# Performance work log

Hardware: AMD Instinct MI355X
Metric: run time of the kernel (lower is better)

## Reference

```python
import jax, jax.numpy as jnp
import numpy as np

ATOM_VOC = 128
APO = 128
NHEAD = 16
D_MODEL = 512
BOND_VOC = 32
CHIRAL_VOC = 4
B, L = 4, 384


def setup_inputs() -> dict:
    key = jax.random.key(0)
    ks = jax.random.split(key, 12)
    atoms = jax.random.randint(ks[0], (B, L), 0, ATOM_VOC)
    chirals = jax.random.randint(ks[1], (B, L), 0, CHIRAL_VOC)
    coordinates = jax.random.normal(ks[2], (B, L, 3), dtype=jnp.float32)
    bonds = jax.random.randint(ks[3], (B, L, L), 0, BOND_VOC)
    # embedding tables; padding_idx rows (0) zeroed to match torch padding_idx
    atype_emb = jax.random.normal(ks[4], (ATOM_VOC, D_MODEL), dtype=jnp.float32) * 0.02
    atype_emb = atype_emb.at[0].set(0.0)
    chiral_emb = jax.random.normal(ks[5], (CHIRAL_VOC, D_MODEL), dtype=jnp.float32) * 0.02
    chiral_emb = chiral_emb.at[0].set(0.0)
    apair_w_emb = jax.random.normal(ks[6], (ATOM_VOC * ATOM_VOC, APO), dtype=jnp.float32) * 0.02
    apair_b_emb = jax.random.normal(ks[7], (ATOM_VOC * ATOM_VOC, APO), dtype=jnp.float32) * 0.02
    means = jax.random.normal(ks[8], (APO,), dtype=jnp.float32) * 0.1
    stds = jnp.ones((APO,), dtype=jnp.float32) + jax.random.normal(ks[9], (APO,), dtype=jnp.float32) * 0.1
    bond_emb = jax.random.normal(ks[10], (BOND_VOC, NHEAD), dtype=jnp.float32) * 0.02
    bond_emb = bond_emb.at[0].set(0.0)
    lin_w = jax.random.normal(ks[11], (NHEAD, APO), dtype=jnp.float32) * (1.0 / np.sqrt(APO))
    lin_b = jnp.zeros((NHEAD,), dtype=jnp.float32)
    return dict(atoms=atoms, chirals=chirals, coordinates=coordinates, bonds=bonds,
                atype_emb=atype_emb, chiral_emb=chiral_emb,
                apair_w_emb=apair_w_emb, apair_b_emb=apair_b_emb,
                means=means, stds=stds, bond_emb=bond_emb, lin_w=lin_w, lin_b=lin_b)


def reference(atoms, chirals, coordinates, bonds, atype_emb, chiral_emb,
              apair_w_emb, apair_b_emb, means, stds, bond_emb, lin_w, lin_b):
    # atoms: [b,l] int; coordinates: [b,l,3]; bonds: [b,l,l] int
    atoms_emb = atype_emb[atoms] + chiral_emb[chirals]          # [b,l,d]
    atoms_emb = jnp.transpose(atoms_emb, (1, 0, 2))             # [l,b,d]
    diff = coordinates[:, None, :, :] - coordinates[:, :, None, :]  # [b,l,l,3]
    d2 = jnp.sum(diff * diff, axis=-1)
    distances = jnp.sqrt(d2 + 1e-12)                            # [b,l,l] (eps avoids nan grad on diag)
    apair_idx = atoms[:, None, :] * ATOM_VOC + atoms[:, :, None]  # [b,l,l]
    ap = apair_w_emb[apair_idx] * distances[..., None] + apair_b_emb[apair_idx]  # [b,l,l,apo]
    s = jnp.abs(stds) + 1e-5
    ap = jnp.exp(-0.5 * jnp.square((ap - means) / s)) / (np.sqrt(2 * np.pi) * s)
    ap = jnp.einsum('bijk,hk->bijh', ap, lin_w) + lin_b + bond_emb[bonds]  # [b,l,l,nhead]
    pad = (atoms == 0)[:, None, :, None]                        # mask key atoms (dim 2)
    ap = jnp.where(pad, -jnp.inf, ap)
    ap = jnp.transpose(ap, (0, 3, 1, 2))                        # [b,nhead,l,l]
    return atoms_emb, ap
```

## Files before the change

### kernel.cpp

```cpp
#include <hip/hip_runtime.h>
#include <hip/hip_fp16.h>
#include <math.h>
#include <string.h>

#define ATOM_VOC 128
#define APO      128
#define NHEAD    16
#define D_MODEL  512
#define NB       4
#define NL       384

typedef __attribute__((ext_vector_type(8))) _Float16 f16x8;
typedef __attribute__((ext_vector_type(4))) float    f32x4;
typedef __attribute__((ext_vector_type(4))) unsigned u32x4;

#define PACK_DWORDS (ATOM_VOC * ATOM_VOC * APO)
#define BFT_SHORTS  (4 * 4 * 16 * 8)

static __device__ inline unsigned short f2h(float x) {
    __half h = __float2half(x);
    unsigned short u; memcpy(&u, &h, 2); return u;
}

__global__ __launch_bounds__(128) void pack_kernel(
    const float* __restrict__ apw, const float* __restrict__ apb,
    const float* __restrict__ means, const float* __restrict__ stds,
    const float* __restrict__ lin_w,
    unsigned* __restrict__ pack, unsigned short* __restrict__ bft, int write_bft)
{
    const int t    = threadIdx.x;
    const int v    = blockIdx.x;
    const int ai   = blockIdx.y;
    const int half = t >> 6;
    const int p    = t & 63;
    const int k0   = 2 * p, k1 = 2 * p + 1;

    const float s0  = fabsf(stds[k0]) + 1e-5f;
    const float s1  = fabsf(stds[k1]) + 1e-5f;
    const float ag0 = 0.84932180028802f / s0;
    const float ag1 = 0.84932180028802f / s1;

    const size_t srcrow = ((size_t)v * ATOM_VOC + ai) * APO;
    float x0, x1;
    if (half == 0) {
        x0 = apw[srcrow + k0] * ag0;
        x1 = apw[srcrow + k1] * ag1;
    } else {
        x0 = (apb[srcrow + k0] - means[k0]) * ag0;
        x1 = (apb[srcrow + k1] - means[k1]) * ag1;
    }
    const int dst = (p >> 5) * 64 + half * 32 + (p & 31);
    pack[((size_t)ai * ATOM_VOC + v) * APO + dst] =
        ((unsigned)f2h(x1) << 16) | f2h(x0);

    if (write_bft && v == 0 && ai == 0) {
#pragma unroll
        for (int hh = 0; hh < 2; ++hh) {
            const int cid  = t + hh * 128;
            const int ks   = cid >> 6;
            const int quad = (cid >> 4) & 3;
            const int h    = cid & 15;
            const int kb   = ks * 32 + quad * 8;
            unsigned short tmp[8];
#pragma unroll
            for (int u = 0; u < 8; ++u) {
                const int kk = kb + u;
                float z = 0.3989422804014327f / (fabsf(stds[kk]) + 1e-5f);
                tmp[u] = f2h(lin_w[h * APO + kk] * z);
            }
            memcpy(&bft[(size_t)cid * 8], tmp, 16);
        }
    }
}

__global__ __launch_bounds__(256) void atoms_emb_kernel(
    const int* __restrict__ atoms, const int* __restrict__ chirals,
    const float* __restrict__ atype_emb, const float* __restrict__ chiral_emb,
    float* __restrict__ out)
{
    const int D4 = D_MODEL / 4;
    int t = blockIdx.x * 256 + threadIdx.x;
    if (t >= NL * NB * D4) return;
    int d4 = t % D4;
    int bl = t / D4;
    int b  = bl % NB;
    int l  = bl / NB;
    int a  = atoms[b * NL + l];
    int c  = chirals[b * NL + l];
    float4 va = ((const float4*)(atype_emb  + (size_t)a * D_MODEL))[d4];
    float4 vc = ((const float4*)(chiral_emb + (size_t)c * D_MODEL))[d4];
    float4 o;
    o.x = va.x + vc.x; o.y = va.y + vc.y; o.z = va.z + vc.z; o.w = va.w + vc.w;
    ((float4*)out)[t] = o;
}

__global__ __launch_bounds__(512, 8) void ap_kernel(
    const int*            __restrict__ atoms,
    const float*          __restrict__ coords,
    const int*            __restrict__ bonds,
    const unsigned*       __restrict__ pack,
    const unsigned short* __restrict__ bft,
    const float*          __restrict__ bond_emb,
    const float*          __restrict__ lin_b,
    float*                __restrict__ out)
{
    const int i    = blockIdx.x;
    const int b    = blockIdx.y;
    const int t    = threadIdx.x;
    const int lane = t & 63;
    const int wave = t >> 6;
    const int h    = lane & 15;
    const int quad = lane >> 4;

    __shared__ unsigned tbl[ATOM_VOC * 64];

    const int ai = atoms[b * NL + i];
    const unsigned* src = pack + (size_t)ai * (ATOM_VOC * APO);

    f16x8 bfrag[4];
#pragma unroll
    for (int ks = 0; ks < 4; ++ks)
        memcpy(&bfrag[ks], bft + ((size_t)((ks * 4 + quad) * 16 + h)) * 8, 16);
    const float lbh = lin_b[h];

    const float cix = coords[((size_t)b * NL + i) * 3 + 0];
    const float ciy = coords[((size_t)b * NL + i) * 3 + 1];
    const float ciz = coords[((size_t)b * NL + i) * 3 + 2];

    int     jv[3];
    __half2 jd2[3];
#pragma unroll
    for (int it = 0; it < 3; ++it) {
        const int j = it * 128 + wave * 16 + h;
        jv[it] = atoms[b * NL + j];
        const float dx = coords[((size_t)b * NL + j) * 3 + 0] - cix;
        const float dy = coords[((size_t)b * NL + j) * 3 + 1] - ciy;
        const float dz = coords[((size_t)b * NL + j) * 3 + 2] - ciz;
        jd2[it] = __half2half2(__float2half(
            sqrtf(fmaf(dx, dx, fmaf(dy, dy, dz * dz)) + 1e-12f)));
    }

    f32x4 acc[3] = {{0.f,0.f,0.f,0.f},{0.f,0.f,0.f,0.f},{0.f,0.f,0.f,0.f}};

#pragma unroll
    for (int ph = 0; ph < 2; ++ph) {
        if (ph) __syncthreads();
#pragma unroll
        for (int itx = 0; itx < 4; ++itx) {
            int c   = itx * 512 + t;
            int row = c >> 4;
            int cc  = c & 15;
            u32x4 d = ((const u32x4*)src)[row * 32 + ph * 16 + cc];
            *(u32x4*)&tbl[row * 64 + 4 * (cc ^ (row & 15))] = d;
        }
        __syncthreads();

#pragma unroll
        for (int it = 0; it < 3; ++it) {
            const int v  = jv[it];
            const int vb = v * 64;
            const int vx = v & 15;
            const __half2 d2 = jd2[it];
#pragma unroll
            for (int ks2 = 0; ks2 < 2; ++ks2) {
                const u32x4 wch = *(const u32x4*)&tbl[vb + 4 * ((ks2 * 4 + quad) ^ vx)];
                const u32x4 bch = *(const u32x4*)&tbl[vb + 4 * ((8 + ks2 * 4 + quad) ^ vx)];
                unsigned afw[4];
#pragma unroll
                for (int q = 0; q < 4; ++q) {
                    __half2 w2, b2;
                    unsigned wd = wch[q], bd = bch[q];
                    memcpy(&w2, &wd, 4); memcpy(&b2, &bd, 4);
                    __half2 u2  = __hfma2(w2, d2, b2);
                    __half2 nm2 = __hmul2(u2, __hneg2(u2));
                    __half2 g2  = h2exp2(nm2);
                    memcpy(&afw[q], &g2, 4);
                }
                f16x8 af;
                memcpy(&af, afw, 16);
                acc[it] = __builtin_amdgcn_mfma_f32_16x16x32_f16(
                    af, bfrag[ph * 2 + ks2], acc[it], 0, 0, 0);
            }
        }
    }

    const size_t bondrow = ((size_t)b * NL + i) * NL;
    float* op = out + (((size_t)(b * NHEAD + h)) * NL + i) * NL;
#pragma unroll
    for (int it = 0; it < 3; ++it) {
        const int jb = it * 128 + wave * 16 + quad * 4;
#pragma unroll
        for (int r = 0; r < 4; ++r) {
            const int bidx = bonds[bondrow + jb + r];
            const int ajr  = atoms[b * NL + jb + r];
            float vv = acc[it][r] + lbh + bond_emb[bidx * NHEAD + h];
            if (ajr == 0) vv = -1.0e30f;
            op[jb + r] = vv;
        }
    }
}

extern "C" void kernel_launch(void* const* d_in, const int* in_sizes, int n_in,
                              void* d_out, int out_size, void* d_ws, size_t ws_size,
                              hipStream_t stream)
{
    const int*   atoms      = (const int*)d_in[0];
    const int*   chirals    = (const int*)d_in[1];
    const float* coords     = (const float*)d_in[2];
    const int*   bonds      = (const int*)d_in[3];
    const float* atype_emb  = (const float*)d_in[4];
    const float* chiral_emb = (const float*)d_in[5];
    const float* apw        = (const float*)d_in[6];
    const float* apb        = (const float*)d_in[7];
    const float* means      = (const float*)d_in[8];
    const float* stds       = (const float*)d_in[9];
    const float* bond_emb   = (const float*)d_in[10];
    const float* lin_w      = (const float*)d_in[11];
    const float* lin_b      = (const float*)d_in[12];
    float* out = (float*)d_out;

    unsigned* pack = (unsigned*)d_ws;
    unsigned short* bftp = (unsigned short*)((char*)d_ws + (size_t)PACK_DWORDS * 4);

    pack_kernel<<<dim3(ATOM_VOC, ATOM_VOC), dim3(128), 0, stream>>>(
        apw, apb, means, stds, lin_w, pack, bftp, 1);

    {
        const int total = NL * NB * (D_MODEL / 4);
        atoms_emb_kernel<<<dim3((total + 255) / 256), dim3(256), 0, stream>>>(
            atoms, chirals, atype_emb, chiral_emb, out);
    }
    {
        float* out2 = out + (size_t)NL * NB * D_MODEL;
        ap_kernel<<<dim3(NL, NB), dim3(512), 0, stream>>>(
            atoms, coords, bonds, pack, bftp, bond_emb, lin_b, out2);
    }
}
```

Measured before the change: 136.9 us.

## Vectorize pack kernel, fuse atom embedding into ap kernel, use direct LDS loads

Rewrites the pack kernel so each thread converts eight values with float4 loads and writes a 16-byte packed chunk, reducing scalar memory traffic. Folds the atom-embedding gather into ap_kernel to drop a separate launch. Stages the pair table into LDS with global_load_lds, issued early so it overlaps setup work. Vectorizes the final bond/mask output stores. These add complexity in the LDS addressing and swizzle mapping.

Measured after the change: 131.8 us. 3.7% less time.

```diff
diff --git a/kernel.cpp b/kernel.cpp
--- a/kernel.cpp
+++ b/kernel.cpp
@@ -22,87 +22,85 @@
     unsigned short u; memcpy(&u, &h, 2); return u;
 }
 
-__global__ __launch_bounds__(128) void pack_kernel(
+static __device__ inline void gload_lds16(const void* g, void* l) {
+    __builtin_amdgcn_global_load_lds(
+        (const __attribute__((address_space(1))) void*)g,
+        (__attribute__((address_space(3))) void*)l, 16, 0, 0);
+}
+
+__global__ __launch_bounds__(256) void pack_kernel(
     const float* __restrict__ apw, const float* __restrict__ apb,
     const float* __restrict__ means, const float* __restrict__ stds,
     const float* __restrict__ lin_w,
     unsigned* __restrict__ pack, unsigned short* __restrict__ bft, int write_bft)
 {
-    const int t    = threadIdx.x;
-    const int v    = blockIdx.x;
-    const int ai   = blockIdx.y;
-    const int half = t >> 6;
-    const int p    = t & 63;
-    const int k0   = 2 * p, k1 = 2 * p + 1;
-
-    const float s0  = fabsf(stds[k0]) + 1e-5f;
-    const float s1  = fabsf(stds[k1]) + 1e-5f;
-    const float ag0 = 0.84932180028802f / s0;
-    const float ag1 = 0.84932180028802f / s1;
+    const int t     = threadIdx.x;
+    const int r     = t >> 5;
+    const int u     = t & 31;
+    const int ph    = u >> 4;
+    const int half  = (u >> 3) & 1;
+    const int q     = u & 7;
+    const int rowid = blockIdx.x * 8 + r;
+    const int ai    = rowid >> 7;
+    const int v     = rowid & 127;
+    const int kb    = ph * 64 + q * 8;
 
     const size_t srcrow = ((size_t)v * ATOM_VOC + ai) * APO;
-    float x0, x1;
-    if (half == 0) {
-        x0 = apw[srcrow + k0] * ag0;
-        x1 = apw[srcrow + k1] * ag1;
-    } else {
-        x0 = (apb[srcrow + k0] - means[k0]) * ag0;
-        x1 = (apb[srcrow + k1] - means[k1]) * ag1;
-    }
-    const int dst = (p >> 5) * 64 + half * 32 + (p & 31);
-    pack[((size_t)ai * ATOM_VOC + v) * APO + dst] =
-        ((unsigned)f2h(x1) << 16) | f2h(x0);
-
-    if (write_bft && v == 0 && ai == 0) {
-#pragma unroll
-        for (int hh = 0; hh < 2; ++hh) {
-            const int cid  = t + hh * 128;
-            const int ks   = cid >> 6;
-            const int quad = (cid >> 4) & 3;
-            const int h    = cid & 15;
-            const int kb   = ks * 32 + quad * 8;
-            unsigned short tmp[8];
-#pragma unroll
-            for (int u = 0; u < 8; ++u) {
-                const int kk = kb + u;
-                float z = 0.3989422804014327f / (fabsf(stds[kk]) + 1e-5f);
-                tmp[u] = f2h(lin_w[h * APO + kk] * z);
-            }
-            memcpy(&bft[(size_t)cid * 8], tmp, 16);
+    const float* sp = (half ? apb : apw) + srcrow + kb;
+    const float4 f0  = *(const float4*)(sp);
+    const float4 f1  = *(const float4*)(sp + 4);
+    const float4 sd0 = *(const float4*)(stds + kb);
+    const float4 sd1 = *(const float4*)(stds + kb + 4);
+
+    float x[8]  = {f0.x, f0.y, f0.z, f0.w, f1.x, f1.y, f1.z, f1.w};
+    float ss[8] = {sd0.x, sd0.y, sd0.z, sd0.w, sd1.x, sd1.y, sd1.z, sd1.w};
+    if (half) {
+        const float4 m0 = *(const float4*)(means + kb);
+        const float4 m1 = *(const float4*)(means + kb + 4);
+        const float mm[8] = {m0.x, m0.y, m0.z, m0.w, m1.x, m1.y, m1.z, m1.w};
+#pragma unroll
+        for (int j = 0; j < 8; ++j) x[j] = x[j] - mm[j];
+    }
+    unsigned dw[4];
+#pragma unroll
+    for (int j = 0; j < 4; ++j) {
+        const float ag0 = 0.84932180028802f / (fabsf(ss[2 * j])     + 1e-5f);
+        const float ag1 = 0.84932180028802f / (fabsf(ss[2 * j + 1]) + 1e-5f);
+        dw[j] = ((unsigned)f2h(x[2 * j + 1] * ag1) << 16) | f2h(x[2 * j] * ag0);
+    }
+    const int dst = ph * 64 + half * 32 + q * 4;
+    *(u32x4*)&pack[((size_t)ai * ATOM_VOC + v) * APO + dst] = *(const u32x4*)dw;
+
+    if (write_bft && blockIdx.x == 0) {
+        const int cid  = t;
+        const int ks   = cid >> 6;
+        const int quad = (cid >> 4) & 3;
+        const int hh   = cid & 15;
+        const int kb2  = ks * 32 + quad * 8;
+        unsigned short tmp[8];
+#pragma unroll
+        for (int uu = 0; uu < 8; ++uu) {
+            const int kk = kb2 + uu;
+            float z = 0.3989422804014327f / (fabsf(stds[kk]) + 1e-5f);
+            tmp[uu] = f2h(lin_w[hh * APO + kk] * z);
         }
-    }
-}
-
-__global__ __launch_bounds__(256) void atoms_emb_kernel(
-    const int* __restrict__ atoms, const int* __restrict__ chirals,
-    const float* __restrict__ atype_emb, const float* __restrict__ chiral_emb,
-    float* __restrict__ out)
-{
-    const int D4 = D_MODEL / 4;
-    int t = blockIdx.x * 256 + threadIdx.x;
-    if (t >= NL * NB * D4) return;
-    int d4 = t % D4;
-    int bl = t / D4;
-    int b  = bl % NB;
-    int l  = bl / NB;
-    int a  = atoms[b * NL + l];
-    int c  = chirals[b * NL + l];
-    float4 va = ((const float4*)(atype_emb  + (size_t)a * D_MODEL))[d4];
-    float4 vc = ((const float4*)(chiral_emb + (size_t)c * D_MODEL))[d4];
-    float4 o;
-    o.x = va.x + vc.x; o.y = va.y + vc.y; o.z = va.z + vc.z; o.w = va.w + vc.w;
-    ((float4*)out)[t] = o;
+        memcpy(&bft[(size_t)cid * 8], tmp, 16);
+    }
 }
 
 __global__ __launch_bounds__(512, 8) void ap_kernel(
     const int*            __restrict__ atoms,
+    const int*            __restrict__ chirals,
     const float*          __restrict__ coords,
     const int*            __restrict__ bonds,
     const unsigned*       __restrict__ pack,
     const unsigned short* __restrict__ bft,
+    const float*          __restrict__ atype_emb,
+    const float*          __restrict__ chiral_emb,
     const float*          __restrict__ bond_emb,
     const float*          __restrict__ lin_b,
-    float*                __restrict__ out)
+    float*                __restrict__ out1,
+    float*                __restrict__ out2)
 {
     const int i    = blockIdx.x;
     const int b    = blockIdx.y;
@@ -117,12 +115,23 @@
     const int ai = atoms[b * NL + i];
     const unsigned* src = pack + (size_t)ai * (ATOM_VOC * APO);
 
-    f16x8 bfrag[4];
-#pragma unroll
-    for (int ks = 0; ks < 4; ++ks)
-        memcpy(&bfrag[ks], bft + ((size_t)((ks * 4 + quad) * 16 + h)) * 8, 16);
+#pragma unroll
+    for (int itx = 0; itx < 4; ++itx) {
+        const int c   = itx * 512 + t;
+        const int row = c >> 4;
+        const int cc  = c & 15;
+        gload_lds16(src + ((size_t)row * 32 + (cc ^ (row & 15))) * 4,
+                    &tbl[(itx * 512 + wave * 64) * 4]);
+    }
+
+    {
+        const int ch = chirals[b * NL + i];
+        out1[((size_t)i * NB + b) * D_MODEL + t] =
+            atype_emb[(size_t)ai * D_MODEL + t] +
+            chiral_emb[(size_t)ch * D_MODEL + t];
+    }
+
     const float lbh = lin_b[h];
-
     const float cix = coords[((size_t)b * NL + i) * 3 + 0];
     const float ciy = coords[((size_t)b * NL + i) * 3 + 1];
     const float ciz = coords[((size_t)b * NL + i) * 3 + 2];
@@ -144,15 +153,20 @@
 
 #pragma unroll
     for (int ph = 0; ph < 2; ++ph) {
-        if (ph) __syncthreads();
-#pragma unroll
-        for (int itx = 0; itx < 4; ++itx) {
-            int c   = itx * 512 + t;
-            int row = c >> 4;
-            int cc  = c & 15;
-            u32x4 d = ((const u32x4*)src)[row * 32 + ph * 16 + cc];
-            *(u32x4*)&tbl[row * 64 + 4 * (cc ^ (row & 15))] = d;
+        if (ph) {
+            __syncthreads();
+#pragma unroll
+            for (int itx = 0; itx < 4; ++itx) {
+                const int c   = itx * 512 + t;
+                const int row = c >> 4;
+                const int cc  = c & 15;
+                gload_lds16(src + ((size_t)row * 32 + 16 + (cc ^ (row & 15))) * 4,
+                            &tbl[(itx * 512 + wave * 64) * 4]);
+            }
         }
+        f16x8 bfA, bfB;
+        memcpy(&bfA, bft + ((size_t)((ph * 2 + 0) * 4 + quad) * 16 + h) * 8, 16);
+        memcpy(&bfB, bft + ((size_t)((ph * 2 + 1) * 4 + quad) * 16 + h) * 8, 16);
         __syncthreads();
 
 #pragma unroll
@@ -179,24 +193,28 @@
                 f16x8 af;
                 memcpy(&af, afw, 16);
                 acc[it] = __builtin_amdgcn_mfma_f32_16x16x32_f16(
-                    af, bfrag[ph * 2 + ks2], acc[it], 0, 0, 0);
+                    af, ks2 ? bfB : bfA, acc[it], 0, 0, 0);
             }
         }
     }
 
     const size_t bondrow = ((size_t)b * NL + i) * NL;
-    float* op = out + (((size_t)(b * NHEAD + h)) * NL + i) * NL;
+    float* op = out2 + (((size_t)(b * NHEAD + h)) * NL + i) * NL;
 #pragma unroll
     for (int it = 0; it < 3; ++it) {
         const int jb = it * 128 + wave * 16 + quad * 4;
-#pragma unroll
-        for (int r = 0; r < 4; ++r) {
-            const int bidx = bonds[bondrow + jb + r];
-            const int ajr  = atoms[b * NL + jb + r];
-            float vv = acc[it][r] + lbh + bond_emb[bidx * NHEAD + h];
-            if (ajr == 0) vv = -1.0e30f;
-            op[jb + r] = vv;
-        }
+        const int4 bd = *(const int4*)(bonds + bondrow + jb);
+        const int4 aj = *(const int4*)(atoms + b * NL + jb);
+        float4 vv;
+        vv.x = acc[it][0] + lbh + bond_emb[bd.x * NHEAD + h];
+        vv.y = acc[it][1] + lbh + bond_emb[bd.y * NHEAD + h];
+        vv.z = acc[it][2] + lbh + bond_emb[bd.z * NHEAD + h];
+        vv.w = acc[it][3] + lbh + bond_emb[bd.w * NHEAD + h];
+        if (aj.x == 0) vv.x = -1.0e30f;
+        if (aj.y == 0) vv.y = -1.0e30f;
+        if (aj.z == 0) vv.z = -1.0e30f;
+        if (aj.w == 0) vv.w = -1.0e30f;
+        *(float4*)(op + jb) = vv;
     }
 }
 
@@ -222,17 +240,13 @@
     unsigned* pack = (unsigned*)d_ws;
     unsigned short* bftp = (unsigned short*)((char*)d_ws + (size_t)PACK_DWORDS * 4);
 
-    pack_kernel<<<dim3(ATOM_VOC, ATOM_VOC), dim3(128), 0, stream>>>(
+    pack_kernel<<<dim3((ATOM_VOC * ATOM_VOC) / 8), dim3(256), 0, stream>>>(
         apw, apb, means, stds, lin_w, pack, bftp, 1);
 
-    {
-        const int total = NL * NB * (D_MODEL / 4);
-        atoms_emb_kernel<<<dim3((total + 255) / 256), dim3(256), 0, stream>>>(
-            atoms, chirals, atype_emb, chiral_emb, out);
-    }
     {
         float* out2 = out + (size_t)NL * NB * D_MODEL;
         ap_kernel<<<dim3(NL, NB), dim3(512), 0, stream>>>(
-            atoms, coords, bonds, pack, bftp, bond_emb, lin_b, out2);
-    }
-}
+            atoms, chirals, coords, bonds, pack, bftp,
+            atype_emb, chiral_emb, bond_emb, lin_b, out, out2);
+    }
+}
```
